# Kernel tuning notes

Hardware: AMD Instinct MI355X
Metric: run time of the kernel (lower is better)

The kernel has to match this reference:

```python
import jax, jax.numpy as jnp
import numpy as np


def setup_inputs() -> dict:
    key = jax.random.key(0)
    ks = jax.random.split(key, 5)
    B, T, C = 4, 2048, 768
    return {
        "x": jax.random.normal(ks[0], (B, T, C), dtype=jnp.float32),
        "w_attn": jax.random.normal(ks[1], (C, 3 * C), dtype=jnp.float32) * 0.02,
        "b_attn": jax.random.normal(ks[2], (3 * C,), dtype=jnp.float32) * 0.02,
        "w_proj": jax.random.normal(ks[3], (C, C), dtype=jnp.float32) * 0.02,
        "b_proj": jax.random.normal(ks[4], (C,), dtype=jnp.float32) * 0.02,
    }


N_HEAD = 8
SOFTMAX_EPS = 1e-6  # the CUDA kernel divides by (sum + 1e-6)


def reference(x, w_attn, b_attn, w_proj, b_proj):
    B, T, C = x.shape
    H = N_HEAD
    hs = C // H
    scale = 1.0 / np.sqrt(hs).astype(np.float32)

    qkv = x @ w_attn + b_attn                      # [B, T, 3C]
    q, k, v = jnp.split(qkv, 3, axis=-1)           # each [B, T, C]
    # reorder to [B, H, T, hs] (matches fused_reorder_qkv)
    def heads(t):
        return t.reshape(B, T, H, hs).transpose(0, 2, 1, 3)
    q, k, v = heads(q), heads(k), heads(v)

    att = jnp.einsum('bhqd,bhkd->bhqk', q, k) * scale
    causal = jnp.tril(jnp.ones((T, T), dtype=bool))  # [T, T]
    att = jnp.where(causal, att, -jnp.inf)
    # kernel softmax: exp(x - max) / (sum + eps)
    m = jnp.max(att, axis=-1, keepdims=True)
    e = jnp.exp(att - m)
    att = e / (jnp.sum(e, axis=-1, keepdims=True) + SOFTMAX_EPS)

    y = jnp.einsum('bhqk,bhkd->bhqd', att, v)      # [B, H, T, hs]
    y = y.transpose(0, 2, 1, 3).reshape(B, T, C)   # fused_reorder_output
    return y @ w_proj + b_proj
```

## Files before the change

### kernel.cpp

```cpp
#include <hip/hip_runtime.h>

constexpr int Bn = 4;
constexpr int Tn = 2048;
constexpr int Cn = 768;
constexpr int Hn = 8;
constexpr int HSn = 96;
constexpr int MR = Bn * Tn;
constexpr int NQKV = 3 * Cn;

typedef __attribute__((ext_vector_type(8))) short bf16x8;
typedef __attribute__((ext_vector_type(4))) float f32x4;

__device__ inline short f2bf(float f) {
  union { float f; unsigned u; } cv; cv.f = f;
  unsigned u = cv.u;
  u += 0x7fffu + ((u >> 16) & 1u);
  return (short)(u >> 16);
}

__device__ inline void gload_lds16(const short* g, short* l) {
  __builtin_amdgcn_global_load_lds(
      (const __attribute__((address_space(1))) unsigned*)g,
      (__attribute__((address_space(3))) unsigned*)l, 16, 0, 0);
}

__global__ __launch_bounds__(256) void cvt_bf16(const float* __restrict__ in,
                                                short* __restrict__ out) {
  const size_t i = ((size_t)blockIdx.x * 256 + threadIdx.x) * 8;
  float4 a = *(const float4*)(in + i);
  float4 b = *(const float4*)(in + i + 4);
  bf16x8 o;
  o[0] = f2bf(a.x); o[1] = f2bf(a.y); o[2] = f2bf(a.z); o[3] = f2bf(a.w);
  o[4] = f2bf(b.x); o[5] = f2bf(b.y); o[6] = f2bf(b.z); o[7] = f2bf(b.w);
  *(bf16x8*)(out + i) = o;
}

__global__ __launch_bounds__(256) void transpose_bf16(
    const float* __restrict__ W, short* __restrict__ Wt, int K, int N) {
  __shared__ float t[32][33];
  const int n0 = blockIdx.x * 32, k0 = blockIdx.y * 32;
  const int tx = threadIdx.x & 31, ty = threadIdx.x >> 5;
  #pragma unroll
  for (int i = 0; i < 32; i += 8)
    t[ty + i][tx] = W[(size_t)(k0 + ty + i) * N + n0 + tx];
  __syncthreads();
  #pragma unroll
  for (int i = 0; i < 32; i += 8)
    Wt[(size_t)(n0 + ty + i) * K + k0 + tx] = f2bf(t[tx][ty + i]);
}

template <bool BF16OUT>
__global__ __launch_bounds__(256) void gemm_mfma(
    const short* __restrict__ A, const short* __restrict__ Bt,
    const float* __restrict__ bias, float* __restrict__ Cf,
    short* __restrict__ Cb, int M, int N, int K, int nxTiles,
    int scale_cols, float scale) {
  __shared__ short As[128 * 32];
  __shared__ short Bs[128 * 32];

  const int cpx = gridDim.x >> 3;
  const int lin = blockIdx.x;
  const int remap = (lin & 7) * cpx + (lin >> 3);
  const int bxt = remap % nxTiles, byt = remap / nxTiles;

  const int tid  = threadIdx.x;
  const int wave = tid >> 6, lane = tid & 63;
  const int bm = byt * 128, bn = bxt * 128;
  const int wr = wave >> 1, wc = wave & 1;
  const int g = lane >> 4, c = lane & 15;

  f32x4 acc[4][4] = {};

  for (int k0 = 0; k0 < K; k0 += 32) {
    __syncthreads();
    #pragma unroll
    for (int cc = 0; cc < 2; ++cc) {
      const int chunkbase = (wave * 2 + cc) * 64;
      const int chunk = chunkbase + lane;
      const int row = chunk >> 2, col16 = chunk & 3;
      gload_lds16(A + (size_t)(bm + row) * K + k0 + col16 * 8,
                  &As[chunkbase * 8]);
      gload_lds16(Bt + (size_t)(bn + row) * K + k0 + col16 * 8,
                  &Bs[chunkbase * 8]);
    }
    __syncthreads();

    bf16x8 af[4], bfr[4];
    #pragma unroll
    for (int m = 0; m < 4; ++m)
      af[m] = *(const bf16x8*)&As[(wr * 64 + m * 16 + c) * 32 + g * 8];
    #pragma unroll
    for (int n = 0; n < 4; ++n)
      bfr[n] = *(const bf16x8*)&Bs[(wc * 64 + n * 16 + c) * 32 + g * 8];
    #pragma unroll
    for (int m = 0; m < 4; ++m)
      #pragma unroll
      for (int n = 0; n < 4; ++n)
        acc[m][n] = __builtin_amdgcn_mfma_f32_16x16x32_bf16(af[m], bfr[n], acc[m][n], 0, 0, 0);
  }

  #pragma unroll
  for (int n = 0; n < 4; ++n) {
    const int col = bn + wc * 64 + n * 16 + c;
    const float bs = bias[col];
    const float sc = (BF16OUT && col < scale_cols) ? scale : 1.f;
    #pragma unroll
    for (int m = 0; m < 4; ++m) {
      #pragma unroll
      for (int r = 0; r < 4; ++r) {
        const int row = bm + wr * 64 + m * 16 + g * 4 + r;
        const float v = acc[m][n][r] + bs;
        if (BF16OUT) Cb[(size_t)row * N + col] = f2bf(v * sc);
        else         Cf[(size_t)row * N + col] = v;
      }
    }
  }
}

__global__ __launch_bounds__(256) void attn_mfma(
    const short* __restrict__ qkv, short* __restrict__ y) {
  __shared__ short Ks[2][64][104];
  __shared__ short Vt[2][96][72];
  __shared__ short Pl[4][16][72];

  const int bid = blockIdx.x;
  const int xcd = bid & 7, jj = bid >> 3;
  const int p = xcd + 8 * (jj >> 4);
  const int bx = jj & 15;
  const int b = p >> 3, h = p & 7;

  const int tid  = threadIdx.x;
  const int wave = tid >> 6;
  const int lane = tid & 63;
  const int g = lane >> 4;
  const int c = lane & 15;

  int buf = 0;

  for (int phase = 0; phase < 2; ++phase) {
    const int qt = phase ? (31 - bx) : bx;
    const int q0 = qt * 64 + wave * 16;

    bf16x8 qf[3];
    {
      const size_t qb = ((size_t)(b * Tn + q0 + c)) * NQKV + h * HSn;
      #pragma unroll
      for (int kk = 0; kk < 3; ++kk)
        qf[kk] = *(const bf16x8*)(qkv + qb + kk * 32 + g * 8);
    }

    f32x4 yacc[6] = {};
    float mrow[4] = {-1e30f, -1e30f, -1e30f, -1e30f};
    float lrow[4] = {};

    bf16x8 kreg[3], vreg[3];
    #pragma unroll
    for (int t = 0; t < 3; ++t) {
      const int i = tid + 256 * t;
      const int kr = i / 12, kc = i % 12;
      kreg[t] = *(const bf16x8*)(
          qkv + ((size_t)(b * Tn + kr)) * NQKV + Cn + h * HSn + kc * 8);
      const int vr = i & 63, vc = i >> 6;
      vreg[t] = *(const bf16x8*)(
          qkv + ((size_t)(b * Tn + vr)) * NQKV + 2 * Cn + h * HSn + vc * 8);
    }

    for (int kt = 0; kt <= qt; ++kt) {
      #pragma unroll
      for (int t = 0; t < 3; ++t) {
        const int i = tid + 256 * t;
        const int kr = i / 12, kc = i % 12;
        *(bf16x8*)&Ks[buf][kr][kc * 8] = kreg[t];
        const int vr = i & 63, vc = i >> 6;
        #pragma unroll
        for (int u = 0; u < 8; ++u) Vt[buf][vc * 8 + u][vr] = vreg[t][u];
      }
      __syncthreads();

      if (kt < qt) {
        const int k0n = (kt + 1) * 64;
        #pragma unroll
        for (int t = 0; t < 3; ++t) {
          const int i = tid + 256 * t;
          const int kr = i / 12, kc = i % 12;
          kreg[t] = *(const bf16x8*)(
              qkv + ((size_t)(b * Tn + k0n + kr)) * NQKV + Cn + h * HSn + kc * 8);
          const int vr = i & 63, vc = i >> 6;
          vreg[t] = *(const bf16x8*)(
              qkv + ((size_t)(b * Tn + k0n + vr)) * NQKV + 2 * Cn + h * HSn + vc * 8);
        }
      }

      const int k0 = kt * 64;

      f32x4 s[4] = {};
      __builtin_amdgcn_s_setprio(1);
      #pragma unroll
      for (int kk = 0; kk < 3; ++kk) {
        #pragma unroll
        for (int t = 0; t < 4; ++t) {
          bf16x8 kf = *(const bf16x8*)&Ks[buf][16 * t + c][32 * kk + g * 8];
          s[t] = __builtin_amdgcn_mfma_f32_16x16x32_bf16(qf[kk], kf, s[t], 0, 0, 0);
        }
      }
      __builtin_amdgcn_s_setprio(0);
      if (kt == qt) {
        #pragma unroll
        for (int t = 0; t < 4; ++t)
          #pragma unroll
          for (int r = 0; r < 4; ++r)
            if (k0 + 16 * t + c > q0 + 4 * g + r) s[t][r] = -1e30f;
      }

      #pragma unroll
      for (int r = 0; r < 4; ++r) {
        float mx = fmaxf(fmaxf(s[0][r], s[1][r]), fmaxf(s[2][r], s[3][r]));
        mx = fmaxf(mx, __shfl_xor(mx, 1));
        mx = fmaxf(mx, __shfl_xor(mx, 2));
        mx = fmaxf(mx, __shfl_xor(mx, 4));
        mx = fmaxf(mx, __shfl_xor(mx, 8));
        const float mnew = fmaxf(mrow[r], mx);
        const float corr = __expf(mrow[r] - mnew);
        mrow[r] = mnew;
        lrow[r] *= corr;
        #pragma unroll
        for (int dt = 0; dt < 6; ++dt) yacc[dt][r] *= corr;
        float ls = 0.f;
        #pragma unroll
        for (int t = 0; t < 4; ++t) {
          const float pv = __expf(s[t][r] - mnew);
          ls += pv;
          Pl[wave][4 * g + r][16 * t + c] = f2bf(pv);
        }
        lrow[r] += ls;
      }

      __builtin_amdgcn_s_setprio(1);
      #pragma unroll
      for (int ks = 0; ks < 2; ++ks) {
        bf16x8 pf = *(const bf16x8*)&Pl[wave][c][ks * 32 + g * 8];
        #pragma unroll
        for (int dt = 0; dt < 6; ++dt) {
          bf16x8 vf = *(const bf16x8*)&Vt[buf][16 * dt + c][ks * 32 + g * 8];
          yacc[dt] = __builtin_amdgcn_mfma_f32_16x16x32_bf16(pf, vf, yacc[dt], 0, 0, 0);
        }
      }
      __builtin_amdgcn_s_setprio(0);

      buf ^= 1;
    }

    #pragma unroll
    for (int r = 0; r < 4; ++r) {
      float v = lrow[r];
      v += __shfl_xor(v, 1);
      v += __shfl_xor(v, 2);
      v += __shfl_xor(v, 4);
      v += __shfl_xor(v, 8);
      lrow[r] = 1.f / (v + 1e-6f);
    }
    #pragma unroll
    for (int dt = 0; dt < 6; ++dt)
      #pragma unroll
      for (int r = 0; r < 4; ++r)
        y[((size_t)(b * Tn + q0 + 4 * g + r)) * Cn + h * HSn + 16 * dt + c] =
            f2bf(yacc[dt][r] * lrow[r]);
  }
}

extern "C" void kernel_launch(void* const* d_in, const int* in_sizes, int n_in,
                              void* d_out, int out_size, void* d_ws, size_t ws_size,
                              hipStream_t stream) {
  const float* x      = (const float*)d_in[0];
  const float* w_attn = (const float*)d_in[1];
  const float* b_attn = (const float*)d_in[2];
  const float* w_proj = (const float*)d_in[3];
  const float* b_proj = (const float*)d_in[4];
  float* out = (float*)d_out;

  size_t off = 0;
  short* qkv = (short*)((char*)d_ws + off); off += (size_t)MR * NQKV * 2;
  short* xb  = (short*)((char*)d_ws + off); off += (size_t)MR * Cn * 2;
  short* yb  = (short*)((char*)d_ws + off); off += (size_t)MR * Cn * 2;
  short* wat = (short*)((char*)d_ws + off); off += (size_t)Cn * NQKV * 2;
  short* wpt = (short*)((char*)d_ws + off); off += (size_t)Cn * Cn * 2;
  if (ws_size < off) return;

  const float scale = 0.102062072615966f;

  cvt_bf16<<<(MR * Cn) / (256 * 8), 256, 0, stream>>>(x, xb);
  transpose_bf16<<<dim3(NQKV / 32, Cn / 32), 256, 0, stream>>>(w_attn, wat, Cn, NQKV);
  transpose_bf16<<<dim3(Cn / 32, Cn / 32), 256, 0, stream>>>(w_proj, wpt, Cn, Cn);

  gemm_mfma<true><<<(NQKV / 128) * (MR / 128), 256, 0, stream>>>(
      xb, wat, b_attn, nullptr, qkv, MR, NQKV, Cn, NQKV / 128, Cn, scale);

  attn_mfma<<<512, 256, 0, stream>>>(qkv, yb);

  gemm_mfma<false><<<(Cn / 128) * (MR / 128), 256, 0, stream>>>(
      yb, wpt, b_proj, out, nullptr, MR, Cn, Cn, Cn / 128, 0, 1.f);
}
```

Baseline: 162.4 us.

## Pre-transpose V into a tiled buffer and stream K via direct-to-LDS loads

Adds a separate kernel that transposes each 64-row V tile into a contiguous per-head tiled buffer, reusing the x bf16 workspace. Attention then reads V fragments straight from global memory into registers, with no LDS transpose. K tiles are fetched with global_load_lds into a swizzled LDS layout for double buffering, so the register staging and scalar LDS stores go away. The softmax switches to exp2 with log2(e) folded into the Q scale. The cost is an extra launch plus extra traffic for the V copy, and V fragments are now served by global or L2 latency rather than LDS.

```diff
diff --git a/kernel.cpp b/kernel.cpp
--- a/kernel.cpp
+++ b/kernel.cpp
@@ -49,6 +49,32 @@
     Wt[(size_t)(n0 + ty + i) * K + k0 + tx] = f2bf(t[tx][ty + i]);
 }
 
+__global__ __launch_bounds__(256) void build_vt(
+    const short* __restrict__ qkv, short* __restrict__ vt) {
+  __shared__ short Vl[64][104];
+  const int blk = blockIdx.x;
+  const int kt = blk & 31, bh = blk >> 5;
+  const int b = bh >> 3, h = bh & 7;
+  const int k0 = kt * 64;
+  const int tid = threadIdx.x;
+
+  #pragma unroll
+  for (int i = tid; i < 768; i += 256) {
+    const int r = i / 12, ch = i % 12;
+    *(bf16x8*)&Vl[r][ch * 8] = *(const bf16x8*)(
+        qkv + ((size_t)(b * Tn + k0 + r)) * NQKV + 2 * Cn + h * HSn + ch * 8);
+  }
+  __syncthreads();
+  #pragma unroll
+  for (int i = tid; i < 768; i += 256) {
+    const int d = i >> 3, w = i & 7;
+    bf16x8 o;
+    #pragma unroll
+    for (int u = 0; u < 8; ++u) o[u] = Vl[w * 8 + u][d];
+    *(bf16x8*)(vt + (size_t)blk * 6144 + d * 64 + w * 8) = o;
+  }
+}
+
 template <bool BF16OUT>
 __global__ __launch_bounds__(256) void gemm_mfma(
     const short* __restrict__ A, const short* __restrict__ Bt,
@@ -118,9 +144,9 @@
 }
 
 __global__ __launch_bounds__(256) void attn_mfma(
-    const short* __restrict__ qkv, short* __restrict__ y) {
-  __shared__ short Ks[2][64][104];
-  __shared__ short Vt[2][96][72];
+    const short* __restrict__ qkv, const short* __restrict__ vt,
+    short* __restrict__ y) {
+  __shared__ short Ksub[2][6144];
   __shared__ short Pl[4][16][72];
 
   const int bid = blockIdx.x;
@@ -135,7 +161,9 @@
   const int g = lane >> 4;
   const int c = lane & 15;
 
-  int buf = 0;
+  const int klane = ((c >> 2) * 6 + (g >> 1)) * 64 + (c & 3) * 16 + (g & 1) * 8;
+  const int voff  = c * 64 + g * 8;
+  const short* vtb = vt + (size_t)((b * 8 + h) * 32) * 6144;
 
   for (int phase = 0; phase < 2; ++phase) {
     const int qt = phase ? (31 - bx) : bx;
@@ -149,47 +177,45 @@
         qf[kk] = *(const bf16x8*)(qkv + qb + kk * 32 + g * 8);
     }
 
+    const short* kap[3];
+    #pragma unroll
+    for (int j = 0; j < 3; ++j) {
+      const int ci = (j * 4 + wave) * 64 + lane;
+      const int s = ci >> 3;
+      const int kb = s / 6, db = s - kb * 6;
+      const int r = kb * 4 + ((ci & 7) >> 1);
+      const int d0 = db * 16 + (ci & 1) * 8;
+      kap[j] = qkv + ((size_t)(b * Tn + r)) * NQKV + Cn + h * HSn + d0;
+    }
+    #pragma unroll
+    for (int j = 0; j < 3; ++j) {
+      gload_lds16(kap[j], &Ksub[0][(j * 4 + wave) * 512]);
+      kap[j] += 64 * NQKV;
+    }
+
     f32x4 yacc[6] = {};
     float mrow[4] = {-1e30f, -1e30f, -1e30f, -1e30f};
     float lrow[4] = {};
-
-    bf16x8 kreg[3], vreg[3];
-    #pragma unroll
-    for (int t = 0; t < 3; ++t) {
-      const int i = tid + 256 * t;
-      const int kr = i / 12, kc = i % 12;
-      kreg[t] = *(const bf16x8*)(
-          qkv + ((size_t)(b * Tn + kr)) * NQKV + Cn + h * HSn + kc * 8);
-      const int vr = i & 63, vc = i >> 6;
-      vreg[t] = *(const bf16x8*)(
-          qkv + ((size_t)(b * Tn + vr)) * NQKV + 2 * Cn + h * HSn + vc * 8);
-    }
+    int buf = 0;
 
     for (int kt = 0; kt <= qt; ++kt) {
-      #pragma unroll
-      for (int t = 0; t < 3; ++t) {
-        const int i = tid + 256 * t;
-        const int kr = i / 12, kc = i % 12;
-        *(bf16x8*)&Ks[buf][kr][kc * 8] = kreg[t];
-        const int vr = i & 63, vc = i >> 6;
-        #pragma unroll
-        for (int u = 0; u < 8; ++u) Vt[buf][vc * 8 + u][vr] = vreg[t][u];
-      }
       __syncthreads();
 
       if (kt < qt) {
-        const int k0n = (kt + 1) * 64;
-        #pragma unroll
-        for (int t = 0; t < 3; ++t) {
-          const int i = tid + 256 * t;
-          const int kr = i / 12, kc = i % 12;
-          kreg[t] = *(const bf16x8*)(
-              qkv + ((size_t)(b * Tn + k0n + kr)) * NQKV + Cn + h * HSn + kc * 8);
-          const int vr = i & 63, vc = i >> 6;
-          vreg[t] = *(const bf16x8*)(
-              qkv + ((size_t)(b * Tn + k0n + vr)) * NQKV + 2 * Cn + h * HSn + vc * 8);
+        #pragma unroll
+        for (int j = 0; j < 3; ++j) {
+          gload_lds16(kap[j], &Ksub[buf ^ 1][(j * 4 + wave) * 512]);
+          kap[j] += 64 * NQKV;
         }
       }
+
+      const short* vtile = vtb + (size_t)kt * 6144 + voff;
+      bf16x8 vf[12];
+      #pragma unroll
+      for (int ks = 0; ks < 2; ++ks)
+        #pragma unroll
+        for (int dt = 0; dt < 6; ++dt)
+          vf[ks * 6 + dt] = *(const bf16x8*)(vtile + dt * 1024 + ks * 32);
 
       const int k0 = kt * 64;
 
@@ -199,7 +225,7 @@
       for (int kk = 0; kk < 3; ++kk) {
         #pragma unroll
         for (int t = 0; t < 4; ++t) {
-          bf16x8 kf = *(const bf16x8*)&Ks[buf][16 * t + c][32 * kk + g * 8];
+          bf16x8 kf = *(const bf16x8*)&Ksub[buf][klane + (24 * t + 2 * kk) * 64];
           s[t] = __builtin_amdgcn_mfma_f32_16x16x32_bf16(qf[kk], kf, s[t], 0, 0, 0);
         }
       }
@@ -220,7 +246,7 @@
         mx = fmaxf(mx, __shfl_xor(mx, 4));
         mx = fmaxf(mx, __shfl_xor(mx, 8));
         const float mnew = fmaxf(mrow[r], mx);
-        const float corr = __expf(mrow[r] - mnew);
+        const float corr = exp2f(mrow[r] - mnew);
         mrow[r] = mnew;
         lrow[r] *= corr;
         #pragma unroll
@@ -228,7 +254,7 @@
         float ls = 0.f;
         #pragma unroll
         for (int t = 0; t < 4; ++t) {
-          const float pv = __expf(s[t][r] - mnew);
+          const float pv = exp2f(s[t][r] - mnew);
           ls += pv;
           Pl[wave][4 * g + r][16 * t + c] = f2bf(pv);
         }
@@ -240,10 +266,8 @@
       for (int ks = 0; ks < 2; ++ks) {
         bf16x8 pf = *(const bf16x8*)&Pl[wave][c][ks * 32 + g * 8];
         #pragma unroll
-        for (int dt = 0; dt < 6; ++dt) {
-          bf16x8 vf = *(const bf16x8*)&Vt[buf][16 * dt + c][ks * 32 + g * 8];
-          yacc[dt] = __builtin_amdgcn_mfma_f32_16x16x32_bf16(pf, vf, yacc[dt], 0, 0, 0);
-        }
+        for (int dt = 0; dt < 6; ++dt)
+          yacc[dt] = __builtin_amdgcn_mfma_f32_16x16x32_bf16(pf, vf[ks * 6 + dt], yacc[dt], 0, 0, 0);
       }
       __builtin_amdgcn_s_setprio(0);
 
@@ -285,8 +309,9 @@
   short* wat = (short*)((char*)d_ws + off); off += (size_t)Cn * NQKV * 2;
   short* wpt = (short*)((char*)d_ws + off); off += (size_t)Cn * Cn * 2;
   if (ws_size < off) return;
-
-  const float scale = 0.102062072615966f;
+  short* vt = xb;
+
+  const float scale = 0.102062072615966f * 1.4426950408889634f;
 
   cvt_bf16<<<(MR * Cn) / (256 * 8), 256, 0, stream>>>(x, xb);
   transpose_bf16<<<dim3(NQKV / 32, Cn / 32), 256, 0, stream>>>(w_attn, wat, Cn, NQKV);
@@ -295,7 +320,9 @@
   gemm_mfma<true><<<(NQKV / 128) * (MR / 128), 256, 0, stream>>>(
       xb, wat, b_attn, nullptr, qkv, MR, NQKV, Cn, NQKV / 128, Cn, scale);
 
-  attn_mfma<<<512, 256, 0, stream>>>(qkv, yb);
+  build_vt<<<Bn * Hn * 32, 256, 0, stream>>>(qkv, vt);
+
+  attn_mfma<<<512, 256, 0, stream>>>(qkv, vt, yb);
 
   gemm_mfma<false><<<(Cn / 128) * (MR / 128), 256, 0, stream>>>(
       yb, wpt, b_proj, out, nullptr, MR, Cn, Cn, Cn / 128, 0, 1.f);
```

After: 200.5 us. 1.23x slower.
